# Optimization experiments

Measured on AMD Instinct MI355X. Metric: run time of the kernel, lower is better.

The kernel has to match this reference:

```python
import jax, jax.numpy as jnp
import numpy as np

B, L, S, D_MODEL, H = 4, 2048, 2048, 512, 8
E = D_MODEL // H  # head dim = 64


def setup_inputs() -> dict:
    key = jax.random.key(0)
    ks = jax.random.split(key, 11)
    s = 1.0 / np.sqrt(D_MODEL)
    return {
        "queries": jax.random.normal(ks[0], (B, L, D_MODEL), jnp.float32),
        "keys": jax.random.normal(ks[1], (B, S, D_MODEL), jnp.float32),
        "values": jax.random.normal(ks[2], (B, S, D_MODEL), jnp.float32),
        "Wq": jax.random.normal(ks[3], (D_MODEL, D_MODEL), jnp.float32) * s,
        "bq": jnp.zeros((D_MODEL,), jnp.float32),
        "Wk": jax.random.normal(ks[4], (D_MODEL, D_MODEL), jnp.float32) * s,
        "bk": jnp.zeros((D_MODEL,), jnp.float32),
        "Wv": jax.random.normal(ks[5], (D_MODEL, D_MODEL), jnp.float32) * s,
        "bv": jnp.zeros((D_MODEL,), jnp.float32),
        "Wo": jax.random.normal(ks[6], (D_MODEL, D_MODEL), jnp.float32) * s,
        "bo": jnp.zeros((D_MODEL,), jnp.float32),
    }


def reference(queries, keys, values, Wq, bq, Wk, bk, Wv, bv, Wo, bo):
    # QKV projections, then split heads: [B, T, H, E]
    q = (queries @ Wq + bq).reshape(B, L, H, E)
    k = (keys @ Wk + bk).reshape(B, S, H, E)
    v = (values @ Wv + bv).reshape(B, S, H, E)
    scale = 1.0 / np.sqrt(E)
    # Naive full attention: materialized [B, H, L, S] scores (as in original)
    scores = jnp.einsum('blhe,bshe->bhls', q, k)
    A = jax.nn.softmax(scale * scores, axis=-1)  # dropout = identity at eval
    out = jnp.einsum('bhls,bshd->blhd', A, v).reshape(B, L, H * E)
    return out @ Wo + bo
```

## Files before the change

### kernel.cpp

```cpp
#include <hip/hip_runtime.h>
#include <hip/hip_bf16.h>


typedef __attribute__((ext_vector_type(8))) short bf8_t;
typedef __attribute__((ext_vector_type(4))) float f4_t;
typedef __attribute__((ext_vector_type(16))) float f16_t;
typedef __attribute__((ext_vector_type(4))) unsigned int u32x4;

#define D_MODEL 512
#define HEADS 8
#define EDIM 64
#define LSEQ 2048
#define NBATCH 4
#define MTOT (NBATCH * LSEQ)
#define N4 (MTOT * D_MODEL / 4)

static __device__ __forceinline__ unsigned short f2bf(float f) {
  union { float f; unsigned int u; } x;
  x.f = f;
  unsigned int u = x.u;
  u += 0x7FFFu + ((u >> 16) & 1u);
  return (unsigned short)(u >> 16);
}

static __device__ __forceinline__ unsigned int pack2bf(float a, float b) {
  union { __hip_bfloat162 h; unsigned int u; } c;
  c.h.x = __float2bfloat16(a);
  c.h.y = __float2bfloat16(b);
  return c.u;
}

__global__ void cvt_all(const float* __restrict__ q, const float* __restrict__ k,
                        const float* __restrict__ v,
                        unsigned short* __restrict__ Xq, unsigned short* __restrict__ Xk,
                        unsigned short* __restrict__ Xv) {
  int i = blockIdx.x * blockDim.x + threadIdx.x;
  int which = i >> 20;
  int idx = i & (N4 - 1);
  const float* in = (which == 0) ? q : (which == 1) ? k : v;
  unsigned short* out = (which == 0) ? Xq : (which == 1) ? Xk : Xv;
  float4 x = ((const float4*)in)[idx];
  ushort4 o;
  o.x = f2bf(x.x); o.y = f2bf(x.y); o.z = f2bf(x.z); o.w = f2bf(x.w);
  ((ushort4*)out)[idx] = o;
}

__global__ void wt_cvt_all(const float* __restrict__ Wq, const float* __restrict__ Wk,
                           const float* __restrict__ Wv, const float* __restrict__ Wo,
                           unsigned short* __restrict__ Wqt, unsigned short* __restrict__ Wkt,
                           unsigned short* __restrict__ Wvt, unsigned short* __restrict__ Wot) {
  __shared__ float tile[64][65];
  const int which = blockIdx.z;
  const float* W = (which == 0) ? Wq : (which == 1) ? Wk : (which == 2) ? Wv : Wo;
  unsigned short* Wt = (which == 0) ? Wqt : (which == 1) ? Wkt : (which == 2) ? Wvt : Wot;
  const int k0 = blockIdx.x * 64, n0 = blockIdx.y * 64;
  const int tx = threadIdx.x & 63;
  const int ty = threadIdx.x >> 6;
#pragma unroll
  for (int i = 0; i < 64; i += 4)
    tile[i + ty][tx] = W[(size_t)(k0 + i + ty) * D_MODEL + n0 + tx];
  __syncthreads();
#pragma unroll
  for (int i = 0; i < 64; i += 4)
    Wt[(size_t)(n0 + i + ty) * D_MODEL + k0 + tx] = f2bf(tile[tx][i + ty]);
}

__device__ __forceinline__ void gemm_core(const unsigned short* __restrict__ A,
                                          const unsigned short* __restrict__ Bt,
                                          unsigned short* lA, unsigned short* lB,
                                          f4_t (&acc)[2][4], int m0, int n0) {
  const int t = threadIdx.x;
  const int lane = t & 63;
  const int w = t >> 6;
  const int wr = w >> 1, wc = w & 1;
  const int r = lane & 15, g = lane >> 4;

  for (int k0 = 0; k0 < D_MODEL; k0 += 32) {
    {
      int rowA = t >> 2, cbA = (t & 3) * 16;
      const char* ga = (const char*)(A + (size_t)(m0 + rowA) * D_MODEL + k0) + cbA;
      __builtin_amdgcn_global_load_lds((const __attribute__((address_space(1))) void*)ga,
                                       (__attribute__((address_space(3))) void*)((char*)lA + t * 16),
                                       16, 0, 0);
#pragma unroll
      for (int ii = 0; ii < 2; ++ii) {
        int c = t + ii * 256;
        int rowB = c >> 2, cbB = (c & 3) * 16;
        const char* gb = (const char*)(Bt + (size_t)(n0 + rowB) * D_MODEL + k0) + cbB;
        __builtin_amdgcn_global_load_lds((const __attribute__((address_space(1))) void*)gb,
                                         (__attribute__((address_space(3))) void*)((char*)lB + c * 16),
                                         16, 0, 0);
      }
    }
    __syncthreads();

    bf8_t af[2], bfv[4];
#pragma unroll
    for (int mi = 0; mi < 2; ++mi)
      af[mi] = *(const bf8_t*)(lA + (wr * 32 + mi * 16 + r) * 32 + g * 8);
#pragma unroll
    for (int ni = 0; ni < 4; ++ni)
      bfv[ni] = *(const bf8_t*)(lB + (wc * 64 + ni * 16 + r) * 32 + g * 8);
#pragma unroll
    for (int mi = 0; mi < 2; ++mi)
#pragma unroll
      for (int ni = 0; ni < 4; ++ni)
        acc[mi][ni] = __builtin_amdgcn_mfma_f32_16x16x32_bf16(af[mi], bfv[ni], acc[mi][ni], 0, 0, 0);
    __syncthreads();
  }
}

#define QSCALE 0.18033688011112042f
__global__ __launch_bounds__(256, 4) void qkv_gemm(
    const unsigned short* __restrict__ Xq, const unsigned short* __restrict__ Xk,
    const unsigned short* __restrict__ Xv, const unsigned short* __restrict__ Wqt,
    const unsigned short* __restrict__ Wkt, const unsigned short* __restrict__ Wvt,
    const float* __restrict__ bq, const float* __restrict__ bk, const float* __restrict__ bv,
    unsigned short* __restrict__ Qh, unsigned short* __restrict__ Kh,
    unsigned short* __restrict__ Vt) {
  __shared__ alignas(16) unsigned short lA[64 * 32];
  __shared__ alignas(16) unsigned short lB[128 * 32];
  const int z = blockIdx.z;
  const unsigned short* A  = (z == 0) ? Xq : (z == 1) ? Xk : Xv;
  const unsigned short* Bt = (z == 0) ? Wqt : (z == 1) ? Wkt : Wvt;
  const float* bias        = (z == 0) ? bq : (z == 1) ? bk : bv;
  const int m0 = blockIdx.x * 64, n0 = blockIdx.y * 128;

  f4_t acc[2][4] = {};
  gemm_core(A, Bt, lA, lB, acc, m0, n0);

  const int lane = threadIdx.x & 63;
  const int w = threadIdx.x >> 6;
  const int wr = w >> 1, wc = w & 1;
  const int r = lane & 15, g = lane >> 4;
#pragma unroll
  for (int mi = 0; mi < 2; ++mi)
#pragma unroll
    for (int ni = 0; ni < 4; ++ni) {
      const int coln = n0 + wc * 64 + ni * 16 + r;
      const float bv_ = bias[coln];
      const int h = coln >> 6, e = coln & 63;
#pragma unroll
      for (int j = 0; j < 4; ++j) {
        const int rowm = m0 + wr * 32 + mi * 16 + g * 4 + j;
        const int b = rowm >> 11, li = rowm & 2047;
        float v = acc[mi][ni][j] + bv_;
        if (z == 0) {
          v *= QSCALE;
          Qh[(((size_t)(b * HEADS + h) * LSEQ + li) << 6) + e] = f2bf(v);
        } else if (z == 1) {
          Kh[(((size_t)(b * HEADS + h) * LSEQ + li) << 6) + e] = f2bf(v);
        } else {
          Vt[(((size_t)(b * HEADS + h) * EDIM + e) << 11) + li] = f2bf(v);
        }
      }
    }
}

__global__ __launch_bounds__(256, 4) void o_gemm(const unsigned short* __restrict__ A,
                                                 const unsigned short* __restrict__ Bt,
                                                 const float* __restrict__ bias,
                                                 float* __restrict__ Cout) {
  __shared__ alignas(16) unsigned short lA[64 * 32];
  __shared__ alignas(16) unsigned short lB[128 * 32];
  const int m0 = blockIdx.x * 64, n0 = blockIdx.y * 128;
  f4_t acc[2][4] = {};
  gemm_core(A, Bt, lA, lB, acc, m0, n0);

  const int lane = threadIdx.x & 63;
  const int w = threadIdx.x >> 6;
  const int wr = w >> 1, wc = w & 1;
  const int r = lane & 15, g = lane >> 4;
#pragma unroll
  for (int mi = 0; mi < 2; ++mi)
#pragma unroll
    for (int ni = 0; ni < 4; ++ni) {
      const int coln = n0 + wc * 64 + ni * 16 + r;
      const float bv_ = bias[coln];
#pragma unroll
      for (int j = 0; j < 4; ++j) {
        const int rowm = m0 + wr * 32 + mi * 16 + g * 4 + j;
        Cout[(size_t)rowm * D_MODEL + coln] = acc[mi][ni][j] + bv_;
      }
    }
}


#define XSTR 68

__device__ __forceinline__ void stage_tile(const unsigned short* __restrict__ Kbase,
                                           const unsigned short* __restrict__ Vbase,
                                           unsigned short* ldsK, unsigned short* ldsV,
                                           int s0, int tg) {
#pragma unroll
  for (int ii = 0; ii < 2; ++ii) {
    int c = tg + ii * 256;
    int row = c >> 3, col = c & 7;
    int colp = col ^ (row & 7);
    const char* gk = (const char*)(Kbase + (size_t)(s0 + row) * EDIM + colp * 8);
    __builtin_amdgcn_global_load_lds((const __attribute__((address_space(1))) void*)gk,
                                     (__attribute__((address_space(3))) void*)((char*)ldsK + c * 16),
                                     16, 0, 0);
    const char* gv = (const char*)(Vbase + (size_t)row * LSEQ + s0 + colp * 8);
    __builtin_amdgcn_global_load_lds((const __attribute__((address_space(1))) void*)gv,
                                     (__attribute__((address_space(3))) void*)((char*)ldsV + c * 16),
                                     16, 0, 0);
  }
}

__global__ __launch_bounds__(512, 4) void flash_attn(const unsigned short* __restrict__ Qh,
                                                     const unsigned short* __restrict__ Kh,
                                                     const unsigned short* __restrict__ Vt,
                                                     unsigned short* __restrict__ Ao) {
  __shared__ alignas(16) unsigned short stg[2][2][2][64 * 64];

  const int t = threadIdx.x;
  const int lane = t & 63;
  const int w = t >> 6;
  const int wg = w >> 2;
  const int wq = w & 3;
  const int tg = t & 255;
  const int qn = lane & 31;
  const int hi = lane >> 5;
  const int bh = blockIdx.y;
  const int q0 = blockIdx.x * 128 + wq * 32;
  const int sbase = wg * (LSEQ / 2);

  bf8_t qf[4];
#pragma unroll
  for (int kst = 0; kst < 4; ++kst)
    qf[kst] = *(const bf8_t*)(Qh + ((size_t)bh * LSEQ + q0 + qn) * EDIM + kst * 16 + hi * 8);

  float l_lane = 0.f;
  f16_t oacc[2];
#pragma unroll
  for (int eh = 0; eh < 2; ++eh)
#pragma unroll
    for (int r = 0; r < 16; ++r) oacc[eh][r] = 0.f;

  const unsigned short* Kbase = Kh + (size_t)bh * LSEQ * EDIM;
  const unsigned short* Vbase = Vt + (size_t)bh * EDIM * LSEQ;

  stage_tile(Kbase, Vbase, stg[wg][0][0], stg[wg][0][1], sbase, tg);
  __syncthreads();

  int cur = 0;
  const int NT = LSEQ / 2 / 64;
  for (int kt = 0; kt < NT; ++kt) {
    if (kt + 1 < NT)
      stage_tile(Kbase, Vbase, stg[wg][cur ^ 1][0], stg[wg][cur ^ 1][1],
                 sbase + (kt + 1) * 64, tg);

    const unsigned short* lsK = stg[wg][cur][0];
    const unsigned short* lsV = stg[wg][cur][1];

    bf8_t kf[2][4];
#pragma unroll
    for (int sh = 0; sh < 2; ++sh)
#pragma unroll
      for (int kst = 0; kst < 4; ++kst) {
        const int row = 32 * sh + qn;
        const int ch = (2 * kst + hi) ^ (row & 7);
        kf[sh][kst] = *(const bf8_t*)(&lsK[row * 64 + ch * 8]);
      }
    f16_t sacc[2];
#pragma unroll
    for (int sh = 0; sh < 2; ++sh)
#pragma unroll
      for (int r = 0; r < 16; ++r) sacc[sh][r] = 0.f;
#pragma unroll
    for (int sh = 0; sh < 2; ++sh)
#pragma unroll
      for (int kst = 0; kst < 4; ++kst)
        sacc[sh] = __builtin_amdgcn_mfma_f32_32x32x16_bf16(kf[sh][kst], qf[kst], sacc[sh], 0, 0, 0);

    unsigned int pk[16];
#pragma unroll
    for (int sh = 0; sh < 2; ++sh)
#pragma unroll
      for (int i = 0; i < 8; ++i) {
        const float a = __builtin_amdgcn_exp2f(sacc[sh][2 * i]);
        const float b = __builtin_amdgcn_exp2f(sacc[sh][2 * i + 1]);
        l_lane += a + b;
        pk[sh * 8 + i] = pack2bf(a, b);
      }

    unsigned int sw[16];
#pragma unroll
    for (int i = 0; i < 16; ++i) sw[i] = __shfl_xor(pk[i], 32);

    bf8_t pvb[4];
#pragma unroll
    for (int t2 = 0; t2 < 4; ++t2) {
      union { u32x4 u; bf8_t b; } pb;
      pb.u[0] = hi ? sw[4 * t2 + 2] : pk[4 * t2 + 0];
      pb.u[1] = hi ? sw[4 * t2 + 3] : pk[4 * t2 + 1];
      pb.u[2] = hi ? pk[4 * t2 + 2] : sw[4 * t2 + 0];
      pb.u[3] = hi ? pk[4 * t2 + 3] : sw[4 * t2 + 1];
      pvb[t2] = pb.b;
    }

#pragma unroll
    for (int eh = 0; eh < 2; ++eh)
#pragma unroll
      for (int t2 = 0; t2 < 4; ++t2) {
        const int row = 32 * eh + qn;
        const int ch = (2 * t2 + hi) ^ (row & 7);
        const bf8_t vf = *(const bf8_t*)(&lsV[row * 64 + ch * 8]);
        oacc[eh] = __builtin_amdgcn_mfma_f32_32x32x16_bf16(vf, pvb[t2], oacc[eh], 0, 0, 0);
      }

    __syncthreads();
    cur ^= 1;
  }

  const float l_own = l_lane + __shfl_xor(l_lane, 32);
  float* xO = (float*)&stg[0][0][0][0];
  float* xL = xO + 128 * XSTR;

  if (wg == 1) {
#pragma unroll
    for (int eh = 0; eh < 2; ++eh)
#pragma unroll
      for (int k = 0; k < 4; ++k) {
        float4 v4;
        v4.x = oacc[eh][4 * k + 0]; v4.y = oacc[eh][4 * k + 1];
        v4.z = oacc[eh][4 * k + 2]; v4.w = oacc[eh][4 * k + 3];
        *(float4*)(xO + (wq * 32 + qn) * XSTR + 32 * eh + 8 * k + 4 * hi) = v4;
      }
    if (hi == 0) xL[wq * 32 + qn] = l_own;
  }
  __syncthreads();

  if (wg == 0) {
    const float inv = 1.f / (l_own + xL[wq * 32 + qn]);
    const int b = bh >> 3, h = bh & 7;
#pragma unroll
    for (int eh = 0; eh < 2; ++eh)
#pragma unroll
      for (int k = 0; k < 4; ++k) {
        const float4 v4 = *(const float4*)(xO + (wq * 32 + qn) * XSTR + 32 * eh + 8 * k + 4 * hi);
        ushort4 ov;
        ov.x = f2bf((oacc[eh][4 * k + 0] + v4.x) * inv);
        ov.y = f2bf((oacc[eh][4 * k + 1] + v4.y) * inv);
        ov.z = f2bf((oacc[eh][4 * k + 2] + v4.z) * inv);
        ov.w = f2bf((oacc[eh][4 * k + 3] + v4.w) * inv);
        const int e = 32 * eh + 8 * k + 4 * hi;
        *(ushort4*)(Ao + ((size_t)(b * LSEQ + q0 + qn)) * D_MODEL + h * EDIM + e) = ov;
      }
  }
}

extern "C" void kernel_launch(void* const* d_in, const int* in_sizes, int n_in,
                              void* d_out, int out_size, void* d_ws, size_t ws_size,
                              hipStream_t stream) {
  const float* queries = (const float*)d_in[0];
  const float* keys    = (const float*)d_in[1];
  const float* values  = (const float*)d_in[2];
  const float* Wq = (const float*)d_in[3];
  const float* bq = (const float*)d_in[4];
  const float* Wk = (const float*)d_in[5];
  const float* bk = (const float*)d_in[6];
  const float* Wv = (const float*)d_in[7];
  const float* bv = (const float*)d_in[8];
  const float* Wo = (const float*)d_in[9];
  const float* bo = (const float*)d_in[10];

  char* ws = (char*)d_ws;
  const size_t XSZ = (size_t)MTOT * D_MODEL * 2;
  unsigned short* Xq  = (unsigned short*)(ws + 0 * XSZ);
  unsigned short* Xk  = (unsigned short*)(ws + 1 * XSZ);
  unsigned short* Xv  = (unsigned short*)(ws + 2 * XSZ);
  unsigned short* Qh  = (unsigned short*)(ws + 3 * XSZ);
  unsigned short* Kh  = (unsigned short*)(ws + 4 * XSZ);
  unsigned short* Vt  = (unsigned short*)(ws + 5 * XSZ);
  unsigned short* Ao  = (unsigned short*)(ws + 6 * XSZ);
  unsigned short* Wqt = (unsigned short*)(ws + 7 * XSZ);
  unsigned short* Wkt = Wqt + 512 * 512;
  unsigned short* Wvt = Wkt + 512 * 512;
  unsigned short* Wot = Wvt + 512 * 512;

  cvt_all<<<3 * N4 / 256, 256, 0, stream>>>(queries, keys, values, Xq, Xk, Xv);
  wt_cvt_all<<<dim3(8, 8, 4), 256, 0, stream>>>(Wq, Wk, Wv, Wo, Wqt, Wkt, Wvt, Wot);

  qkv_gemm<<<dim3(MTOT / 64, D_MODEL / 128, 3), 256, 0, stream>>>(
      Xq, Xk, Xv, Wqt, Wkt, Wvt, bq, bk, bv, Qh, Kh, Vt);

  flash_attn<<<dim3(LSEQ / 128, NBATCH * HEADS), 512, 0, stream>>>(Qh, Kh, Vt, Ao);

  o_gemm<<<dim3(MTOT / 64, D_MODEL / 128), 256, 0, stream>>>(Ao, Wot, bo, (float*)d_out);
}
```

Before: 115.9 us.

## Fuse fp32-to-bf16 input conversion into QKV GEMM and add MFMA priority hints

Drops the separate activation conversion kernel. The QKV GEMM now loads fp32 inputs straight into LDS through an XOR-swizzled layout and packs them to bf16 while reading fragments, which removes a full write and reread of three bf16 activation tensors. The grid is reordered so the N tiles of one M block are launched next to each other, for better reuse of A in cache. In flash attention, s_setprio is raised around the MFMA blocks and the row-sum accumulator is split in two. The trade-off is twice the LDS and global traffic for the A tile inside the GEMM, plus per-iteration conversion ALU work.

```diff
diff --git a/kernel.cpp b/kernel.cpp
--- a/kernel.cpp
+++ b/kernel.cpp
@@ -13,7 +13,6 @@
 #define LSEQ 2048
 #define NBATCH 4
 #define MTOT (NBATCH * LSEQ)
-#define N4 (MTOT * D_MODEL / 4)
 
 static __device__ __forceinline__ unsigned short f2bf(float f) {
   union { float f; unsigned int u; } x;
@@ -28,21 +27,6 @@
   c.h.x = __float2bfloat16(a);
   c.h.y = __float2bfloat16(b);
   return c.u;
-}
-
-__global__ void cvt_all(const float* __restrict__ q, const float* __restrict__ k,
-                        const float* __restrict__ v,
-                        unsigned short* __restrict__ Xq, unsigned short* __restrict__ Xk,
-                        unsigned short* __restrict__ Xv) {
-  int i = blockIdx.x * blockDim.x + threadIdx.x;
-  int which = i >> 20;
-  int idx = i & (N4 - 1);
-  const float* in = (which == 0) ? q : (which == 1) ? k : v;
-  unsigned short* out = (which == 0) ? Xq : (which == 1) ? Xk : Xv;
-  float4 x = ((const float4*)in)[idx];
-  ushort4 o;
-  o.x = f2bf(x.x); o.y = f2bf(x.y); o.z = f2bf(x.z); o.w = f2bf(x.w);
-  ((ushort4*)out)[idx] = o;
 }
 
 __global__ void wt_cvt_all(const float* __restrict__ Wq, const float* __restrict__ Wk,
@@ -65,9 +49,10 @@
     Wt[(size_t)(n0 + i + ty) * D_MODEL + k0 + tx] = f2bf(tile[tx][i + ty]);
 }
 
-__device__ __forceinline__ void gemm_core(const unsigned short* __restrict__ A,
+template <bool AF32>
+__device__ __forceinline__ void gemm_core(const void* __restrict__ Av,
                                           const unsigned short* __restrict__ Bt,
-                                          unsigned short* lA, unsigned short* lB,
+                                          void* __restrict__ lAv, unsigned short* __restrict__ lB,
                                           f4_t (&acc)[2][4], int m0, int n0) {
   const int t = threadIdx.x;
   const int lane = t & 63;
@@ -76,28 +61,58 @@
   const int r = lane & 15, g = lane >> 4;
 
   for (int k0 = 0; k0 < D_MODEL; k0 += 32) {
-    {
+    if constexpr (AF32) {
+      const float* A = (const float*)Av;
+#pragma unroll
+      for (int ii = 0; ii < 2; ++ii) {
+        int c = t + ii * 256;
+        int row = c >> 3, col = c & 7;
+        int colp = col ^ (row & 7);
+        const char* ga = (const char*)(A + (size_t)(m0 + row) * D_MODEL + k0 + colp * 4);
+        __builtin_amdgcn_global_load_lds((const __attribute__((address_space(1))) void*)ga,
+                                         (__attribute__((address_space(3))) void*)((char*)lAv + c * 16),
+                                         16, 0, 0);
+      }
+    } else {
+      const unsigned short* A = (const unsigned short*)Av;
       int rowA = t >> 2, cbA = (t & 3) * 16;
       const char* ga = (const char*)(A + (size_t)(m0 + rowA) * D_MODEL + k0) + cbA;
       __builtin_amdgcn_global_load_lds((const __attribute__((address_space(1))) void*)ga,
-                                       (__attribute__((address_space(3))) void*)((char*)lA + t * 16),
+                                       (__attribute__((address_space(3))) void*)((char*)lAv + t * 16),
                                        16, 0, 0);
-#pragma unroll
-      for (int ii = 0; ii < 2; ++ii) {
-        int c = t + ii * 256;
-        int rowB = c >> 2, cbB = (c & 3) * 16;
-        const char* gb = (const char*)(Bt + (size_t)(n0 + rowB) * D_MODEL + k0) + cbB;
-        __builtin_amdgcn_global_load_lds((const __attribute__((address_space(1))) void*)gb,
-                                         (__attribute__((address_space(3))) void*)((char*)lB + c * 16),
-                                         16, 0, 0);
-      }
+    }
+#pragma unroll
+    for (int ii = 0; ii < 2; ++ii) {
+      int c = t + ii * 256;
+      int rowB = c >> 2, cbB = (c & 3) * 16;
+      const char* gb = (const char*)(Bt + (size_t)(n0 + rowB) * D_MODEL + k0) + cbB;
+      __builtin_amdgcn_global_load_lds((const __attribute__((address_space(1))) void*)gb,
+                                       (__attribute__((address_space(3))) void*)((char*)lB + c * 16),
+                                       16, 0, 0);
     }
     __syncthreads();
 
     bf8_t af[2], bfv[4];
-#pragma unroll
-    for (int mi = 0; mi < 2; ++mi)
-      af[mi] = *(const bf8_t*)(lA + (wr * 32 + mi * 16 + r) * 32 + g * 8);
+    if constexpr (AF32) {
+      const float* lA = (const float*)lAv;
+#pragma unroll
+      for (int mi = 0; mi < 2; ++mi) {
+        const int row = wr * 32 + mi * 16 + r;
+        const f4_t lo = *(const f4_t*)(lA + row * 32 + (((2 * g + 0) ^ (row & 7)) << 2));
+        const f4_t hi4 = *(const f4_t*)(lA + row * 32 + (((2 * g + 1) ^ (row & 7)) << 2));
+        union { unsigned int u[4]; bf8_t b; } pb;
+        pb.u[0] = pack2bf(lo[0], lo[1]);
+        pb.u[1] = pack2bf(lo[2], lo[3]);
+        pb.u[2] = pack2bf(hi4[0], hi4[1]);
+        pb.u[3] = pack2bf(hi4[2], hi4[3]);
+        af[mi] = pb.b;
+      }
+    } else {
+      const unsigned short* lA = (const unsigned short*)lAv;
+#pragma unroll
+      for (int mi = 0; mi < 2; ++mi)
+        af[mi] = *(const bf8_t*)(lA + (wr * 32 + mi * 16 + r) * 32 + g * 8);
+    }
 #pragma unroll
     for (int ni = 0; ni < 4; ++ni)
       bfv[ni] = *(const bf8_t*)(lB + (wc * 64 + ni * 16 + r) * 32 + g * 8);
@@ -112,22 +127,22 @@
 
 #define QSCALE 0.18033688011112042f
 __global__ __launch_bounds__(256, 4) void qkv_gemm(
-    const unsigned short* __restrict__ Xq, const unsigned short* __restrict__ Xk,
-    const unsigned short* __restrict__ Xv, const unsigned short* __restrict__ Wqt,
-    const unsigned short* __restrict__ Wkt, const unsigned short* __restrict__ Wvt,
+    const float* __restrict__ Xq, const float* __restrict__ Xk, const float* __restrict__ Xv,
+    const unsigned short* __restrict__ Wqt, const unsigned short* __restrict__ Wkt,
+    const unsigned short* __restrict__ Wvt,
     const float* __restrict__ bq, const float* __restrict__ bk, const float* __restrict__ bv,
     unsigned short* __restrict__ Qh, unsigned short* __restrict__ Kh,
     unsigned short* __restrict__ Vt) {
-  __shared__ alignas(16) unsigned short lA[64 * 32];
+  __shared__ alignas(16) float lA[64 * 32];
   __shared__ alignas(16) unsigned short lB[128 * 32];
   const int z = blockIdx.z;
-  const unsigned short* A  = (z == 0) ? Xq : (z == 1) ? Xk : Xv;
+  const float* A           = (z == 0) ? Xq : (z == 1) ? Xk : Xv;
   const unsigned short* Bt = (z == 0) ? Wqt : (z == 1) ? Wkt : Wvt;
   const float* bias        = (z == 0) ? bq : (z == 1) ? bk : bv;
-  const int m0 = blockIdx.x * 64, n0 = blockIdx.y * 128;
+  const int n0 = blockIdx.x * 128, m0 = blockIdx.y * 64;
 
   f4_t acc[2][4] = {};
-  gemm_core(A, Bt, lA, lB, acc, m0, n0);
+  gemm_core<true>(A, Bt, lA, lB, acc, m0, n0);
 
   const int lane = threadIdx.x & 63;
   const int w = threadIdx.x >> 6;
@@ -163,9 +178,9 @@
                                                  float* __restrict__ Cout) {
   __shared__ alignas(16) unsigned short lA[64 * 32];
   __shared__ alignas(16) unsigned short lB[128 * 32];
-  const int m0 = blockIdx.x * 64, n0 = blockIdx.y * 128;
+  const int n0 = blockIdx.x * 128, m0 = blockIdx.y * 64;
   f4_t acc[2][4] = {};
-  gemm_core(A, Bt, lA, lB, acc, m0, n0);
+  gemm_core<false>(A, Bt, lA, lB, acc, m0, n0);
 
   const int lane = threadIdx.x & 63;
   const int w = threadIdx.x >> 6;
@@ -184,7 +199,6 @@
       }
     }
 }
-
 
 #define XSTR 68
 
@@ -231,7 +245,7 @@
   for (int kst = 0; kst < 4; ++kst)
     qf[kst] = *(const bf8_t*)(Qh + ((size_t)bh * LSEQ + q0 + qn) * EDIM + kst * 16 + hi * 8);
 
-  float l_lane = 0.f;
+  float l0 = 0.f, l1 = 0.f;
   f16_t oacc[2];
 #pragma unroll
   for (int eh = 0; eh < 2; ++eh)
@@ -268,11 +282,13 @@
     for (int sh = 0; sh < 2; ++sh)
 #pragma unroll
       for (int r = 0; r < 16; ++r) sacc[sh][r] = 0.f;
+    __builtin_amdgcn_s_setprio(1);
 #pragma unroll
     for (int sh = 0; sh < 2; ++sh)
 #pragma unroll
       for (int kst = 0; kst < 4; ++kst)
         sacc[sh] = __builtin_amdgcn_mfma_f32_32x32x16_bf16(kf[sh][kst], qf[kst], sacc[sh], 0, 0, 0);
+    __builtin_amdgcn_s_setprio(0);
 
     unsigned int pk[16];
 #pragma unroll
@@ -281,7 +297,7 @@
       for (int i = 0; i < 8; ++i) {
         const float a = __builtin_amdgcn_exp2f(sacc[sh][2 * i]);
         const float b = __builtin_amdgcn_exp2f(sacc[sh][2 * i + 1]);
-        l_lane += a + b;
+        if (sh == 0) l0 += a + b; else l1 += a + b;
         pk[sh * 8 + i] = pack2bf(a, b);
       }
 
@@ -300,6 +316,7 @@
       pvb[t2] = pb.b;
     }
 
+    __builtin_amdgcn_s_setprio(1);
 #pragma unroll
     for (int eh = 0; eh < 2; ++eh)
 #pragma unroll
@@ -309,11 +326,13 @@
         const bf8_t vf = *(const bf8_t*)(&lsV[row * 64 + ch * 8]);
         oacc[eh] = __builtin_amdgcn_mfma_f32_32x32x16_bf16(vf, pvb[t2], oacc[eh], 0, 0, 0);
       }
+    __builtin_amdgcn_s_setprio(0);
 
     __syncthreads();
     cur ^= 1;
   }
 
+  const float l_lane = l0 + l1;
   const float l_own = l_lane + __shfl_xor(l_lane, 32);
   float* xO = (float*)&stg[0][0][0][0];
   float* xL = xO + 128 * XSTR;
@@ -368,9 +387,6 @@
 
   char* ws = (char*)d_ws;
   const size_t XSZ = (size_t)MTOT * D_MODEL * 2;
-  unsigned short* Xq  = (unsigned short*)(ws + 0 * XSZ);
-  unsigned short* Xk  = (unsigned short*)(ws + 1 * XSZ);
-  unsigned short* Xv  = (unsigned short*)(ws + 2 * XSZ);
   unsigned short* Qh  = (unsigned short*)(ws + 3 * XSZ);
   unsigned short* Kh  = (unsigned short*)(ws + 4 * XSZ);
   unsigned short* Vt  = (unsigned short*)(ws + 5 * XSZ);
@@ -380,13 +396,12 @@
   unsigned short* Wvt = Wkt + 512 * 512;
   unsigned short* Wot = Wvt + 512 * 512;
 
-  cvt_all<<<3 * N4 / 256, 256, 0, stream>>>(queries, keys, values, Xq, Xk, Xv);
   wt_cvt_all<<<dim3(8, 8, 4), 256, 0, stream>>>(Wq, Wk, Wv, Wo, Wqt, Wkt, Wvt, Wot);
 
-  qkv_gemm<<<dim3(MTOT / 64, D_MODEL / 128, 3), 256, 0, stream>>>(
-      Xq, Xk, Xv, Wqt, Wkt, Wvt, bq, bk, bv, Qh, Kh, Vt);
+  qkv_gemm<<<dim3(D_MODEL / 128, MTOT / 64, 3), 256, 0, stream>>>(
+      queries, keys, values, Wqt, Wkt, Wvt, bq, bk, bv, Qh, Kh, Vt);
 
   flash_attn<<<dim3(LSEQ / 128, NBATCH * HEADS), 512, 0, stream>>>(Qh, Kh, Vt, Ao);
 
-  o_gemm<<<dim3(MTOT / 64, D_MODEL / 128), 256, 0, stream>>>(Ao, Wot, bo, (float*)d_out);
-}
+  o_gemm<<<dim3(D_MODEL / 128, MTOT / 64), 256, 0, stream>>>(Ao, Wot, bo, (float*)d_out);
+}
```

Measured after the change: 115.5 us. About the same (-0.4%).

## Double-buffer GEMM LDS staging and remap block indices for XCD-local reuse

Applied to the files above, without the earlier changes.

The GEMM core now double-buffers the A and B tiles in LDS, issuing the next k-slice's global-to-LDS loads before computing on the current slice. This replaces two barriers per iteration with one and aims to overlap load latency with MFMA work. The QKV, attention and output kernels switch to 1D grids with a swizzled block-to-tile mapping. The mapping groups blocks that share A rows or the same head onto the same XCD, to improve L2 reuse. In exchange, LDS use doubles, and the launch bounds rise to 6 blocks per CU, which may limit registers.

```diff
diff --git a/kernel.cpp b/kernel.cpp
--- a/kernel.cpp
+++ b/kernel.cpp
@@ -29,6 +29,10 @@
   c.h.y = __float2bfloat16(b);
   return c.u;
 }
+
+#define GLOAD_LDS(gptr, lptr)                                                        \
+  __builtin_amdgcn_global_load_lds((const __attribute__((address_space(1))) void*)(gptr), \
+                                   (__attribute__((address_space(3))) void*)(lptr), 16, 0, 0)
 
 __global__ void cvt_all(const float* __restrict__ q, const float* __restrict__ k,
                         const float* __restrict__ v,
@@ -65,39 +69,54 @@
     Wt[(size_t)(n0 + i + ty) * D_MODEL + k0 + tx] = f2bf(tile[tx][i + ty]);
 }
 
+__device__ __forceinline__ void stage_a(const unsigned short* __restrict__ A,
+                                        unsigned short* lA, int m0, int k0) {
+  const int t = threadIdx.x;
+  int rowA = t >> 2, cbA = (t & 3) * 16;
+  GLOAD_LDS((const char*)(A + (size_t)(m0 + rowA) * D_MODEL + k0) + cbA, (char*)lA + t * 16);
+}
+__device__ __forceinline__ void stage_b(const unsigned short* __restrict__ Bt,
+                                        unsigned short* lB, int n0, int k0) {
+  const int t = threadIdx.x;
+#pragma unroll
+  for (int ii = 0; ii < 2; ++ii) {
+    int c = t + ii * 256;
+    int rowB = c >> 2, cbB = (c & 3) * 16;
+    GLOAD_LDS((const char*)(Bt + (size_t)(n0 + rowB) * D_MODEL + k0) + cbB, (char*)lB + c * 16);
+  }
+}
+
 __device__ __forceinline__ void gemm_core(const unsigned short* __restrict__ A,
                                           const unsigned short* __restrict__ Bt,
-                                          unsigned short* lA, unsigned short* lB,
+                                          unsigned short* __restrict__ lAv,
+                                          unsigned short* __restrict__ lBv,
                                           f4_t (&acc)[2][4], int m0, int n0) {
   const int t = threadIdx.x;
   const int lane = t & 63;
   const int w = t >> 6;
   const int wr = w >> 1, wc = w & 1;
   const int r = lane & 15, g = lane >> 4;
-
-  for (int k0 = 0; k0 < D_MODEL; k0 += 32) {
-    {
-      int rowA = t >> 2, cbA = (t & 3) * 16;
-      const char* ga = (const char*)(A + (size_t)(m0 + rowA) * D_MODEL + k0) + cbA;
-      __builtin_amdgcn_global_load_lds((const __attribute__((address_space(1))) void*)ga,
-                                       (__attribute__((address_space(3))) void*)((char*)lA + t * 16),
-                                       16, 0, 0);
-#pragma unroll
-      for (int ii = 0; ii < 2; ++ii) {
-        int c = t + ii * 256;
-        int rowB = c >> 2, cbB = (c & 3) * 16;
-        const char* gb = (const char*)(Bt + (size_t)(n0 + rowB) * D_MODEL + k0) + cbB;
-        __builtin_amdgcn_global_load_lds((const __attribute__((address_space(1))) void*)gb,
-                                         (__attribute__((address_space(3))) void*)((char*)lB + c * 16),
-                                         16, 0, 0);
-      }
+  const int ASZ = 64 * 32, BSZ = 128 * 32;
+
+  stage_a(A, lAv, m0, 0);
+  stage_b(Bt, lBv, n0, 0);
+  __syncthreads();
+
+  int cur = 0;
+  const int NK = D_MODEL / 32;
+  for (int ks = 0; ks < NK; ++ks) {
+    if (ks + 1 < NK) {
+      const int kn = (ks + 1) * 32;
+      stage_a(A, lAv + (cur ^ 1) * ASZ, m0, kn);
+      stage_b(Bt, lBv + (cur ^ 1) * BSZ, n0, kn);
     }
-    __syncthreads();
 
     bf8_t af[2], bfv[4];
+    const unsigned short* lA = lAv + cur * ASZ;
 #pragma unroll
     for (int mi = 0; mi < 2; ++mi)
       af[mi] = *(const bf8_t*)(lA + (wr * 32 + mi * 16 + r) * 32 + g * 8);
+    const unsigned short* lB = lBv + cur * BSZ;
 #pragma unroll
     for (int ni = 0; ni < 4; ++ni)
       bfv[ni] = *(const bf8_t*)(lB + (wc * 64 + ni * 16 + r) * 32 + g * 8);
@@ -107,27 +126,35 @@
       for (int ni = 0; ni < 4; ++ni)
         acc[mi][ni] = __builtin_amdgcn_mfma_f32_16x16x32_bf16(af[mi], bfv[ni], acc[mi][ni], 0, 0, 0);
     __syncthreads();
+    cur ^= 1;
   }
 }
 
 #define QSCALE 0.18033688011112042f
-__global__ __launch_bounds__(256, 4) void qkv_gemm(
+__global__ __launch_bounds__(256, 6) void qkv_gemm(
     const unsigned short* __restrict__ Xq, const unsigned short* __restrict__ Xk,
-    const unsigned short* __restrict__ Xv, const unsigned short* __restrict__ Wqt,
-    const unsigned short* __restrict__ Wkt, const unsigned short* __restrict__ Wvt,
+    const unsigned short* __restrict__ Xv,
+    const unsigned short* __restrict__ Wqt, const unsigned short* __restrict__ Wkt,
+    const unsigned short* __restrict__ Wvt,
     const float* __restrict__ bq, const float* __restrict__ bk, const float* __restrict__ bv,
     unsigned short* __restrict__ Qh, unsigned short* __restrict__ Kh,
     unsigned short* __restrict__ Vt) {
-  __shared__ alignas(16) unsigned short lA[64 * 32];
-  __shared__ alignas(16) unsigned short lB[128 * 32];
-  const int z = blockIdx.z;
+  __shared__ alignas(16) unsigned short lA[2][64 * 32];
+  __shared__ alignas(16) unsigned short lB[2][128 * 32];
+  const int p = blockIdx.x;
+  const int res = p & 7, q = p >> 3;
+  const int xx = q & 3;
+  const int grp = res + ((q >> 2) << 3);
+  const int z = grp >> 7;
+  const int y = grp & 127;
+  const int n0 = xx * 128, m0 = y * 64;
+
   const unsigned short* A  = (z == 0) ? Xq : (z == 1) ? Xk : Xv;
   const unsigned short* Bt = (z == 0) ? Wqt : (z == 1) ? Wkt : Wvt;
   const float* bias        = (z == 0) ? bq : (z == 1) ? bk : bv;
-  const int m0 = blockIdx.x * 64, n0 = blockIdx.y * 128;
 
   f4_t acc[2][4] = {};
-  gemm_core(A, Bt, lA, lB, acc, m0, n0);
+  gemm_core(A, Bt, &lA[0][0], &lB[0][0], acc, m0, n0);
 
   const int lane = threadIdx.x & 63;
   const int w = threadIdx.x >> 6;
@@ -157,15 +184,20 @@
     }
 }
 
-__global__ __launch_bounds__(256, 4) void o_gemm(const unsigned short* __restrict__ A,
+__global__ __launch_bounds__(256, 6) void o_gemm(const unsigned short* __restrict__ A,
                                                  const unsigned short* __restrict__ Bt,
                                                  const float* __restrict__ bias,
                                                  float* __restrict__ Cout) {
-  __shared__ alignas(16) unsigned short lA[64 * 32];
-  __shared__ alignas(16) unsigned short lB[128 * 32];
-  const int m0 = blockIdx.x * 64, n0 = blockIdx.y * 128;
+  __shared__ alignas(16) unsigned short lA[2][64 * 32];
+  __shared__ alignas(16) unsigned short lB[2][128 * 32];
+  const int p = blockIdx.x;
+  const int res = p & 7, q = p >> 3;
+  const int xx = q & 3;
+  const int grp = res + ((q >> 2) << 3);
+  const int n0 = xx * 128, m0 = grp * 64;
+
   f4_t acc[2][4] = {};
-  gemm_core(A, Bt, lA, lB, acc, m0, n0);
+  gemm_core(A, Bt, &lA[0][0], &lB[0][0], acc, m0, n0);
 
   const int lane = threadIdx.x & 63;
   const int w = threadIdx.x >> 6;
@@ -185,7 +217,6 @@
     }
 }
 
-
 #define XSTR 68
 
 __device__ __forceinline__ void stage_tile(const unsigned short* __restrict__ Kbase,
@@ -197,14 +228,10 @@
     int c = tg + ii * 256;
     int row = c >> 3, col = c & 7;
     int colp = col ^ (row & 7);
-    const char* gk = (const char*)(Kbase + (size_t)(s0 + row) * EDIM + colp * 8);
-    __builtin_amdgcn_global_load_lds((const __attribute__((address_space(1))) void*)gk,
-                                     (__attribute__((address_space(3))) void*)((char*)ldsK + c * 16),
-                                     16, 0, 0);
-    const char* gv = (const char*)(Vbase + (size_t)row * LSEQ + s0 + colp * 8);
-    __builtin_amdgcn_global_load_lds((const __attribute__((address_space(1))) void*)gv,
-                                     (__attribute__((address_space(3))) void*)((char*)ldsV + c * 16),
-                                     16, 0, 0);
+    GLOAD_LDS((const char*)(Kbase + (size_t)(s0 + row) * EDIM + colp * 8),
+              (char*)ldsK + c * 16);
+    GLOAD_LDS((const char*)(Vbase + (size_t)row * LSEQ + s0 + colp * 8),
+              (char*)ldsV + c * 16);
   }
 }
 
@@ -222,8 +249,11 @@
   const int tg = t & 255;
   const int qn = lane & 31;
   const int hi = lane >> 5;
-  const int bh = blockIdx.y;
-  const int q0 = blockIdx.x * 128 + wq * 32;
+  const int p = blockIdx.x;
+  const int xcd = p & 7, jj = p >> 3;
+  const int bh = xcd * 4 + (jj >> 4);
+  const int qblk = jj & 15;
+  const int q0 = qblk * 128 + wq * 32;
   const int sbase = wg * (LSEQ / 2);
 
   bf8_t qf[4];
@@ -383,10 +413,10 @@
   cvt_all<<<3 * N4 / 256, 256, 0, stream>>>(queries, keys, values, Xq, Xk, Xv);
   wt_cvt_all<<<dim3(8, 8, 4), 256, 0, stream>>>(Wq, Wk, Wv, Wo, Wqt, Wkt, Wvt, Wot);
 
-  qkv_gemm<<<dim3(MTOT / 64, D_MODEL / 128, 3), 256, 0, stream>>>(
+  qkv_gemm<<<1536, 256, 0, stream>>>(
       Xq, Xk, Xv, Wqt, Wkt, Wvt, bq, bk, bv, Qh, Kh, Vt);
 
-  flash_attn<<<dim3(LSEQ / 128, NBATCH * HEADS), 512, 0, stream>>>(Qh, Kh, Vt, Ao);
-
-  o_gemm<<<dim3(MTOT / 64, D_MODEL / 128), 256, 0, stream>>>(Ao, Wot, bo, (float*)d_out);
-}
+  flash_attn<<<512, 512, 0, stream>>>(Qh, Kh, Vt, Ao);
+
+  o_gemm<<<512, 256, 0, stream>>>(Ao, Wot, bo, (float*)d_out);
+}
```

New measurement: 109.2 us. 1.06x faster.
